# Kernel tuning notes

Hardware: AMD Instinct MI355X
Metric: run time of the kernel (lower is better)

Reference implementation:

```python
import jax, jax.numpy as jnp
import numpy as np

HIDDEN = 4544
NUM_HEADS = 71
HEAD_DIM = 64
SEQ = 2048
ROPE_BASE = 10000.0


def setup_inputs() -> dict:
    key = jax.random.key(0)
    k1, k2, k3 = jax.random.split(key, 3)
    hidden_states = jax.random.normal(k1, (1, 1, SEQ, HIDDEN), dtype=jnp.float32)
    # additive causal mask (0 on/below diagonal, -1e9 above)
    causal = jnp.tril(jnp.ones((SEQ, SEQ), dtype=bool))
    attention_mask = jnp.where(causal, 0.0, -1e9).astype(jnp.float32)[None, None]
    w_qkv = jax.random.normal(k2, (HIDDEN, (NUM_HEADS + 2) * HEAD_DIM), dtype=jnp.float32) * 0.02
    w_dense = jax.random.normal(k3, (HIDDEN, HIDDEN), dtype=jnp.float32) * 0.02
    # RoPE caches as in TtFalconRotaryEmbedding
    inv_freq = 1.0 / (ROPE_BASE ** (jnp.arange(0, HEAD_DIM, 2, dtype=jnp.float32) / HEAD_DIM))
    t = jnp.arange(SEQ, dtype=jnp.float32)
    freqs = jnp.outer(t, inv_freq)                      # [S, HD/2]
    emb = jnp.concatenate([freqs, freqs], axis=-1)      # [S, HD]
    return {
        "hidden_states": hidden_states,
        "attention_mask": attention_mask,
        "w_qkv": w_qkv,
        "w_dense": w_dense,
        "cos": jnp.cos(emb),
        "sin": jnp.sin(emb),
    }


def _rope(x, cos, sin):
    # x: [..., S, HD]; Falcon rotate_half: cat(-x2, x1)
    x1, x2 = jnp.split(x, 2, axis=-1)
    rot = jnp.concatenate([-x2, x1], axis=-1)
    return x * cos + rot * sin


def reference(hidden_states, attention_mask, w_qkv, w_dense, cos, sin):
    S = hidden_states.shape[2]
    x = hidden_states[0, 0]                              # [S, H]
    qkv = (x @ w_qkv).reshape(S, NUM_HEADS + 2, HEAD_DIM)
    q = jnp.transpose(qkv[:, :NUM_HEADS], (1, 0, 2))     # [nh, S, hd]
    k = qkv[:, NUM_HEADS]                                # [S, hd] (single MQA K head)
    v = qkv[:, NUM_HEADS + 1]                            # [S, hd]
    q = _rope(q, cos[None, :S], sin[None, :S])
    k = _rope(k, cos[:S], sin[:S])
    scale = 1.0 / np.sqrt(HEAD_DIM).astype(np.float32)
    scores = jnp.einsum('hsd,td->hst', q, k) * scale + attention_mask[0, 0][None]
    probs = jax.nn.softmax(scores, axis=-1)              # [nh, S, S]
    ctx = jnp.einsum('hst,td->hsd', probs, v)            # [nh, S, hd]
    out = jnp.transpose(ctx, (1, 0, 2)).reshape(S, NUM_HEADS * HEAD_DIM) @ w_dense
    return out[None, None]                               # [1, 1, S, H]
```

## Files before the change

kernel.cpp:

```cpp
#include <hip/hip_runtime.h>

typedef unsigned short u16;
typedef unsigned int u32;
typedef __attribute__((ext_vector_type(8))) __bf16 bf16x8;
typedef __attribute__((ext_vector_type(4))) float f32x4;

#define SEQ   2048
#define NH    71
#define HD    64
#define HID   4544
#define NQKV  4672
#define KP    4608
#define KSL   1536

__device__ __forceinline__ u16 f2bf(float f) {
    __bf16 b = (__bf16)f;
    return __builtin_bit_cast(u16, b);
}
__device__ __forceinline__ float bf2f(u16 u) {
    __bf16 b = __builtin_bit_cast(__bf16, u);
    return (float)b;
}

__device__ __forceinline__ void gload_lds16(const u16* g, u16* l) {
    __builtin_amdgcn_global_load_lds(
        (const __attribute__((address_space(1))) u32*)g,
        (__attribute__((address_space(3))) u32*)l, 16, 0, 0);
}

__global__ __launch_bounds__(256) void k_convert(const float* __restrict__ in,
                                                 u16* __restrict__ out) {
    const int row = blockIdx.x;
    const float* src = in + (size_t)row * HID;
    u16* dst = out + (size_t)row * KP;
    for (int c = threadIdx.x; c < KP / 8; c += 256) {
        u16 o[8];
        if (c < HID / 8) {
            float4 v0 = *(const float4*)(src + c * 8);
            float4 v1 = *(const float4*)(src + c * 8 + 4);
            o[0] = f2bf(v0.x); o[1] = f2bf(v0.y); o[2] = f2bf(v0.z); o[3] = f2bf(v0.w);
            o[4] = f2bf(v1.x); o[5] = f2bf(v1.y); o[6] = f2bf(v1.z); o[7] = f2bf(v1.w);
        } else {
#pragma unroll
            for (int j = 0; j < 8; ++j) o[j] = 0;
        }
        *(uint4*)(dst + c * 8) = *(uint4*)o;
    }
}

__global__ __launch_bounds__(256) void k_transpose(const float* __restrict__ in,
                                                   u16* __restrict__ out,
                                                   int R, int C, int Rp) {
    __shared__ float tile[32][33];
    int c0 = blockIdx.x * 32, r0 = blockIdx.y * 32;
    int tx = threadIdx.x & 31, ty = threadIdx.x >> 5;
#pragma unroll
    for (int i = 0; i < 32; i += 8) {
        int r = r0 + ty + i, c = c0 + tx;
        tile[ty + i][tx] = (r < R && c < C) ? in[(size_t)r * C + c] : 0.f;
    }
    __syncthreads();
#pragma unroll
    for (int i = 0; i < 32; i += 8)
        out[(size_t)(c0 + ty + i) * Rp + r0 + tx] = f2bf(tile[tx][ty + i]);
}

__global__ __launch_bounds__(512) void k_gemm_sk(const u16* __restrict__ A,
                                                 const u16* __restrict__ BT,
                                                 u16* __restrict__ C0,
                                                 u16* __restrict__ C1,
                                                 u16* __restrict__ C2,
                                                 int N, int ntN) {
    __shared__ u16 ls[4][256 * 64];
    const int tid = threadIdx.x;
    const int lane = tid & 63;
    const int wid = tid >> 6;
    const int wr = wid >> 2, wc = wid & 3;
    const int l15 = lane & 15, lg = lane >> 4;

    const int p = blockIdx.x;
    const int m0 = (p & 7) * 256;
    const int rr_ = p >> 3;
    const int ks = rr_ / ntN;
    const int n0 = (rr_ % ntN) * 256;
    const int k0 = ks * KSL;

    const int sg = lane >> 3;
    const int slot = lane & 7;
    const u16* sb[4];
    int dstoff[4];
#pragma unroll
    for (int i = 0; i < 4; ++i) {
        int r = i * 64 + wid * 8 + sg;
        int sc = slot ^ (r & 7);
        sb[i] = (sc < 4) ? (A  + (size_t)(m0 + r) * KP + k0 + sc * 8)
                         : (BT + (size_t)(n0 + r) * KP + k0 + (sc ^ 4) * 8);
        dstoff[i] = r * 64 + slot * 8;
    }

    f32x4 acc[8][4];
#pragma unroll
    for (int i = 0; i < 8; ++i)
#pragma unroll
        for (int j = 0; j < 4; ++j) acc[i][j] = (f32x4){0.f, 0.f, 0.f, 0.f};

#define STG(d, kt, i) gload_lds16(sb[i] + (size_t)(kt) * 32, &ls[d][dstoff[i]])

    const int NT = KSL / 32;
    STG(0, 0, 0); STG(0, 0, 1); STG(0, 0, 2); STG(0, 0, 3);
    STG(1, 1, 0); STG(1, 1, 1); STG(1, 1, 2); STG(1, 1, 3);
    STG(2, 2, 0); STG(2, 2, 1); STG(2, 2, 2); STG(2, 2, 3);
    asm volatile("s_waitcnt vmcnt(8)" ::: "memory");
    __builtin_amdgcn_s_barrier();

    for (int kt = 0; kt < NT; ++kt) {
        const u16* L = ls[kt & 3];
        const int db = (kt + 3) & 3;
        const bool st = (kt + 3 < NT);
        bf16x8 bfr[4], af[4];
#pragma unroll
        for (int ni = 0; ni < 4; ++ni) {
            int rb = wc * 64 + ni * 16 + l15;
            bfr[ni] = *(const bf16x8*)(L + rb * 64 + ((lg ^ (rb & 7) ^ 4) << 3));
        }
#pragma unroll
        for (int mi = 0; mi < 4; ++mi) {
            int ra = wr * 128 + mi * 16 + l15;
            af[mi] = *(const bf16x8*)(L + ra * 64 + ((lg ^ (ra & 7)) << 3));
        }
        if (st) { STG(db, kt + 3, 0); STG(db, kt + 3, 1); }
        __builtin_amdgcn_s_barrier();
        __builtin_amdgcn_s_setprio(1);
#pragma unroll
        for (int mi = 0; mi < 4; ++mi)
#pragma unroll
            for (int ni = 0; ni < 4; ++ni)
                acc[mi][ni] = __builtin_amdgcn_mfma_f32_16x16x32_bf16(
                    af[mi], bfr[ni], acc[mi][ni], 0, 0, 0);
        __builtin_amdgcn_s_setprio(0);
        __builtin_amdgcn_s_barrier();
#pragma unroll
        for (int mi = 0; mi < 4; ++mi) {
            int ra = wr * 128 + (mi + 4) * 16 + l15;
            af[mi] = *(const bf16x8*)(L + ra * 64 + ((lg ^ (ra & 7)) << 3));
        }
        if (st) { STG(db, kt + 3, 2); STG(db, kt + 3, 3); }
        __builtin_amdgcn_s_barrier();
        __builtin_amdgcn_s_setprio(1);
#pragma unroll
        for (int mi = 0; mi < 4; ++mi)
#pragma unroll
            for (int ni = 0; ni < 4; ++ni)
                acc[mi + 4][ni] = __builtin_amdgcn_mfma_f32_16x16x32_bf16(
                    af[mi], bfr[ni], acc[mi + 4][ni], 0, 0, 0);
        __builtin_amdgcn_s_setprio(0);
        if (kt < NT - 3)       asm volatile("s_waitcnt vmcnt(8)" ::: "memory");
        else if (kt == NT - 3) asm volatile("s_waitcnt vmcnt(4)" ::: "memory");
        else if (kt == NT - 2) asm volatile("s_waitcnt vmcnt(0)" ::: "memory");
        __builtin_amdgcn_s_barrier();
    }
#undef STG

    u16* Cks = (ks == 0) ? C0 : (ks == 1) ? C1 : C2;
#pragma unroll
    for (int mi = 0; mi < 8; ++mi)
#pragma unroll
        for (int ni = 0; ni < 4; ++ni) {
            int row = m0 + wr * 128 + mi * 16 + lg * 4;
            int col = n0 + wc * 64 + ni * 16 + l15;
            if (col < N) {
#pragma unroll
                for (int j = 0; j < 4; ++j)
                    Cks[(size_t)(row + j) * N + col] = f2bf(acc[mi][ni][j]);
            }
        }
}

__global__ __launch_bounds__(256) void k_reduce(const u16* __restrict__ P0,
                                                const u16* __restrict__ P1,
                                                const u16* __restrict__ P2,
                                                float* __restrict__ out, int n8) {
    for (int i = blockIdx.x * 256 + threadIdx.x; i < n8; i += gridDim.x * 256) {
        uint4 a = ((const uint4*)P0)[i];
        uint4 b = ((const uint4*)P1)[i];
        uint4 c = ((const uint4*)P2)[i];
        float r[8];
#pragma unroll
        for (int j = 0; j < 4; ++j) {
            u32 aw = (&a.x)[j], bw = (&b.x)[j], cw = (&c.x)[j];
            r[j * 2]     = bf2f((u16)(aw & 0xffff)) + bf2f((u16)(bw & 0xffff))
                         + bf2f((u16)(cw & 0xffff));
            r[j * 2 + 1] = bf2f((u16)(aw >> 16)) + bf2f((u16)(bw >> 16))
                         + bf2f((u16)(cw >> 16));
        }
        ((float4*)out)[i * 2]     = (float4){r[0], r[1], r[2], r[3]};
        ((float4*)out)[i * 2 + 1] = (float4){r[4], r[5], r[6], r[7]};
    }
}

__global__ __launch_bounds__(256) void k_rope(const u16* __restrict__ P0,
                                              const u16* __restrict__ P1,
                                              const u16* __restrict__ P2,
                                              const float* __restrict__ cosb,
                                              const float* __restrict__ sinb,
                                              u16* __restrict__ qb, u16* __restrict__ kb,
                                              u16* __restrict__ vT) {
    int s = blockIdx.x;
    __shared__ float row[NQKV];
    __shared__ float cs[64], sn[64];
    if (threadIdx.x < 64) {
        cs[threadIdx.x] = cosb[s * 64 + threadIdx.x];
        sn[threadIdx.x] = sinb[s * 64 + threadIdx.x];
    }
    const u16* r0 = P0 + (size_t)s * NQKV;
    const u16* r1 = P1 + (size_t)s * NQKV;
    const u16* r2 = P2 + (size_t)s * NQKV;
    for (int e = threadIdx.x; e < NQKV; e += 256)
        row[e] = bf2f(r0[e]) + bf2f(r1[e]) + bf2f(r2[e]);
    __syncthreads();
    const float qscale = 0.125f * 1.44269504f;
    for (int e = threadIdx.x; e < NQKV; e += 256) {
        int h = e >> 6, d = e & 63;
        float x = row[e];
        if (h < 72) {
            float other = row[h * 64 + ((d < 32) ? d + 32 : d - 32)];
            float rot = (d < 32) ? -other : other;
            float rr = x * cs[d] + rot * sn[d];
            if (h < NH) qb[((size_t)h * SEQ + s) * 64 + d] = f2bf(rr * qscale);
            else        kb[(size_t)s * 64 + d] = f2bf(rr);
        } else {
            vT[(size_t)d * SEQ + s] = f2bf(x);
        }
    }
}

__global__ __launch_bounds__(512) void k_attn(const u16* __restrict__ qb,
                                              const u16* __restrict__ kb,
                                              const u16* __restrict__ vT,
                                              u16* __restrict__ ctx) {
    const int tid = threadIdx.x;
    const int lane = tid & 63;
    const int wid = tid >> 6;
    const int l15 = lane & 15, lg = lane >> 4;

    const int bid = blockIdx.x;
    const int qt = 63 - bid / 9;
    const int hg = bid % 9;
    int h = hg * 8 + wid;
    const bool hval = (h < NH);
    if (!hval) h = NH - 1;
    const int q0 = qt * 32;
    const int nt = (qt >> 2) + 1;

    __shared__ u16 lsK[2][128 * 64];
    __shared__ u16 lsV[2][64 * 128];
    __shared__ u16 lsP[8][32 * 128];
    u16* myP = lsP[wid];

    const int kr = tid >> 3, kc = tid & 7;
    const int vd = tid >> 4, vc = tid & 15;

    bf16x8 qf[2][2];
#pragma unroll
    for (int mi = 0; mi < 2; ++mi)
#pragma unroll
        for (int ks = 0; ks < 2; ++ks)
            qf[mi][ks] = *(const bf16x8*)(qb + ((size_t)h * SEQ + q0 + mi * 16 + l15) * 64
                                          + ks * 32 + lg * 8);

    f32x4 oacc[2][4];
#pragma unroll
    for (int i = 0; i < 2; ++i)
#pragma unroll
        for (int j = 0; j < 4; ++j) oacc[i][j] = (f32x4){0.f, 0.f, 0.f, 0.f};
    float mrun[2] = {-3e38f, -3e38f};
    float lrun[2] = {0.f, 0.f};

    uint4 kg0, kg1, vg0, vg1;
    kg0 = *(const uint4*)(kb + (size_t)kr * 64 + kc * 8);
    kg1 = *(const uint4*)(kb + (size_t)(kr + 64) * 64 + kc * 8);
    vg0 = *(const uint4*)(vT + (size_t)vd * SEQ + vc * 8);
    vg1 = *(const uint4*)(vT + (size_t)(vd + 32) * SEQ + vc * 8);
    {
        const int kswz = (kr & 7) << 4;
        *(uint4*)((char*)lsK[0] + kr * 128 + ((kc * 16) ^ kswz)) = kg0;
        *(uint4*)((char*)lsK[0] + (kr + 64) * 128 + ((kc * 16) ^ kswz)) = kg1;
        *(uint4*)((char*)lsV[0] + vd * 256 + ((vc * 16) ^ ((vd & 15) << 4))) = vg0;
        *(uint4*)((char*)lsV[0] + (vd + 32) * 256 + ((vc * 16) ^ (((vd + 32) & 15) << 4))) = vg1;
    }

    for (int t = 0; t < nt; ++t) {
        const int t0 = t << 7;
        const int cb = t & 1;
        if (t + 1 < nt) {
            const int t1 = t0 + 128;
            kg0 = *(const uint4*)(kb + (size_t)(t1 + kr) * 64 + kc * 8);
            kg1 = *(const uint4*)(kb + (size_t)(t1 + kr + 64) * 64 + kc * 8);
            vg0 = *(const uint4*)(vT + (size_t)vd * SEQ + t1 + vc * 8);
            vg1 = *(const uint4*)(vT + (size_t)(vd + 32) * SEQ + t1 + vc * 8);
        }
        __syncthreads();

        f32x4 sacc[2][8];
#pragma unroll
        for (int i = 0; i < 2; ++i)
#pragma unroll
            for (int j = 0; j < 8; ++j) sacc[i][j] = (f32x4){0.f, 0.f, 0.f, 0.f};
        __builtin_amdgcn_s_setprio(1);
#pragma unroll
        for (int ni = 0; ni < 8; ++ni) {
            const int rr = ni * 16 + l15;
            const int swz = (rr & 7) << 4;
            bf16x8 kf0 = *(const bf16x8*)((const char*)lsK[cb] + rr * 128 + ((lg * 16) ^ swz));
            bf16x8 kf1 = *(const bf16x8*)((const char*)lsK[cb] + rr * 128 + ((64 + lg * 16) ^ swz));
            sacc[0][ni] = __builtin_amdgcn_mfma_f32_16x16x32_bf16(kf0, qf[0][0], sacc[0][ni], 0, 0, 0);
            sacc[1][ni] = __builtin_amdgcn_mfma_f32_16x16x32_bf16(kf0, qf[1][0], sacc[1][ni], 0, 0, 0);
            sacc[0][ni] = __builtin_amdgcn_mfma_f32_16x16x32_bf16(kf1, qf[0][1], sacc[0][ni], 0, 0, 0);
            sacc[1][ni] = __builtin_amdgcn_mfma_f32_16x16x32_bf16(kf1, qf[1][1], sacc[1][ni], 0, 0, 0);
        }
        __builtin_amdgcn_s_setprio(0);
        const bool last = (t == nt - 1);

#pragma unroll
        for (int mi = 0; mi < 2; ++mi) {
            const int q = q0 + mi * 16 + l15;
            if (last) {
#pragma unroll
                for (int ni = 0; ni < 8; ++ni)
#pragma unroll
                    for (int jj = 0; jj < 4; ++jj)
                        if (t0 + ni * 16 + lg * 4 + jj > q) sacc[mi][ni][jj] = -1e9f;
            }
            float m = sacc[mi][0][0];
#pragma unroll
            for (int ni = 0; ni < 8; ++ni)
#pragma unroll
                for (int jj = 0; jj < 4; ++jj) m = fmaxf(m, sacc[mi][ni][jj]);
            m = fmaxf(m, __shfl_xor(m, 16, 64));
            m = fmaxf(m, __shfl_xor(m, 32, 64));
            float mnew = fmaxf(mrun[mi], m);
            const bool skiprs = (__all(mnew - mrun[mi] <= 8.0f) != 0);
            float mref = skiprs ? mrun[mi] : mnew;
            float rs = 0.f;
#pragma unroll
            for (int ni = 0; ni < 8; ++ni)
#pragma unroll
                for (int jj = 0; jj < 4; ++jj) {
                    float pp = exp2f(sacc[mi][ni][jj] - mref);
                    sacc[mi][ni][jj] = pp;
                    rs += pp;
                }
            rs += __shfl_xor(rs, 16, 64);
            rs += __shfl_xor(rs, 32, 64);
            if (skiprs) {
                lrun[mi] += rs;
            } else {
                float alpha = exp2f(mrun[mi] - mnew);
                lrun[mi] = lrun[mi] * alpha + rs;
                mrun[mi] = mnew;
#pragma unroll
                for (int jj = 0; jj < 4; ++jj) {
                    float aB = __shfl(alpha, (lane & 48) + ((lane >> 4) & 3) * 4 + jj, 64);
#pragma unroll
                    for (int nd = 0; nd < 4; ++nd) oacc[mi][nd][jj] *= aB;
                }
            }

            const int qh = mi * 16 + l15;
            const int pswz = (qh & 7) << 4;
#pragma unroll
            for (int ni = 0; ni < 8; ++ni) {
                u32 w0 = (u32)f2bf(sacc[mi][ni][0]) | ((u32)f2bf(sacc[mi][ni][1]) << 16);
                u32 w1 = (u32)f2bf(sacc[mi][ni][2]) | ((u32)f2bf(sacc[mi][ni][3]) << 16);
                uint2 w; w.x = w0; w.y = w1;
                *(uint2*)((char*)myP + qh * 256 + ((ni * 32 + lg * 8) ^ pswz)) = w;
            }
        }

        __builtin_amdgcn_s_setprio(1);
#pragma unroll
        for (int ks = 0; ks < 4; ++ks) {
            bf16x8 pf[2];
#pragma unroll
            for (int mi = 0; mi < 2; ++mi) {
                const int qh = mi * 16 + l15;
                pf[mi] = *(const bf16x8*)((const char*)myP + qh * 256
                                          + ((ks * 64 + lg * 16) ^ ((qh & 7) << 4)));
            }
#pragma unroll
            for (int nd = 0; nd < 4; ++nd) {
                const int rr = nd * 16 + l15;
                bf16x8 vf = *(const bf16x8*)((const char*)lsV[cb] + rr * 256
                                             + ((ks * 64 + lg * 16) ^ ((rr & 15) << 4)));
                oacc[0][nd] = __builtin_amdgcn_mfma_f32_16x16x32_bf16(pf[0], vf, oacc[0][nd], 0, 0, 0);
                oacc[1][nd] = __builtin_amdgcn_mfma_f32_16x16x32_bf16(pf[1], vf, oacc[1][nd], 0, 0, 0);
            }
        }
        __builtin_amdgcn_s_setprio(0);

        if (t + 1 < nt) {
            const int nb = cb ^ 1;
            const int kswz = (kr & 7) << 4;
            *(uint4*)((char*)lsK[nb] + kr * 128 + ((kc * 16) ^ kswz)) = kg0;
            *(uint4*)((char*)lsK[nb] + (kr + 64) * 128 + ((kc * 16) ^ kswz)) = kg1;
            *(uint4*)((char*)lsV[nb] + vd * 256 + ((vc * 16) ^ ((vd & 15) << 4))) = vg0;
            *(uint4*)((char*)lsV[nb] + (vd + 32) * 256 + ((vc * 16) ^ (((vd + 32) & 15) << 4))) = vg1;
        }
    }

    if (hval) {
#pragma unroll
        for (int mi = 0; mi < 2; ++mi)
#pragma unroll
            for (int jj = 0; jj < 4; ++jj) {
                float lB = __shfl(lrun[mi], (lane & 48) + ((lane >> 4) & 3) * 4 + jj, 64);
                float inv = 1.0f / lB;
                int q = q0 + mi * 16 + lg * 4 + jj;
#pragma unroll
                for (int nd = 0; nd < 4; ++nd)
                    ctx[(size_t)q * KP + h * 64 + nd * 16 + l15] = f2bf(oacc[mi][nd][jj] * inv);
            }
    } else {
#pragma unroll
        for (int mi = 0; mi < 2; ++mi)
#pragma unroll
            for (int jj = 0; jj < 4; ++jj) {
                int q = q0 + mi * 16 + lg * 4 + jj;
#pragma unroll
                for (int nd = 0; nd < 4; ++nd)
                    ctx[(size_t)q * KP + HID + nd * 16 + l15] = 0;
            }
    }
}

extern "C" void kernel_launch(void* const* d_in, const int* in_sizes, int n_in,
                              void* d_out, int out_size, void* d_ws, size_t ws_size,
                              hipStream_t stream) {
    const float* hs      = (const float*)d_in[0];
    const float* w_qkv   = (const float*)d_in[2];
    const float* w_dense = (const float*)d_in[3];
    const float* cosb    = (const float*)d_in[4];
    const float* sinb    = (const float*)d_in[5];
    float* out = (float*)d_out;

    char* ws = (char*)d_ws;
    u16*   x_bf  = (u16*)(ws + 0);
    u16*   wT    = (u16*)(ws + 18874368);
    u16*   qP0   = (u16*)(ws + 63700992);
    u16*   qP1   = (u16*)(ws + 82837504);
    u16*   qP2   = (u16*)(ws + 101974016);
    u16*   q_bf  = (u16*)(ws + 121110528);
    u16*   k_bf  = (u16*)(ws + 139722752);
    u16*   vT_bf = (u16*)(ws + 139984896);
    u16*   dP0   = (u16*)(ws + 63700992);
    u16*   dP1   = (u16*)(ws + 82837504);
    u16*   dP2   = (u16*)(ws + 101974016);

    k_convert<<<2048, 256, 0, stream>>>(hs, x_bf);
    k_transpose<<<dim3(152, 144), 256, 0, stream>>>(w_qkv, wT, HID, NQKV, KP);
    k_gemm_sk<<<dim3(456), 512, 0, stream>>>(x_bf, wT, qP0, qP1, qP2, NQKV, 19);
    k_rope<<<SEQ, 256, 0, stream>>>(qP0, qP1, qP2, cosb, sinb, q_bf, k_bf, vT_bf);
    k_attn<<<dim3(576), 512, 0, stream>>>(q_bf, k_bf, vT_bf, x_bf );
    k_transpose<<<dim3(144, 144), 256, 0, stream>>>(w_dense, wT, HID, HID, KP);
    k_gemm_sk<<<dim3(432), 512, 0, stream>>>(x_bf , wT, dP0, dP1, dP2, HID, 18);
    k_reduce<<<2048, 256, 0, stream>>>(dP0, dP1, dP2, out, SEQ * HID / 8);
}
```

Before: 406.9 us.

## Single-buffer K/V tiles and shrink per-wave P scratch in attention kernel

```diff
diff --git a/kernel.cpp b/kernel.cpp
--- a/kernel.cpp
+++ b/kernel.cpp
@@ -252,9 +252,9 @@
     const int q0 = qt * 32;
     const int nt = (qt >> 2) + 1;
 
-    __shared__ u16 lsK[2][128 * 64];
-    __shared__ u16 lsV[2][64 * 128];
-    __shared__ u16 lsP[8][32 * 128];
+    __shared__ u16 lsK[128 * 64];
+    __shared__ u16 lsV[64 * 128];
+    __shared__ u16 lsP[8][16 * 128];
     u16* myP = lsP[wid];
 
     const int kr = tid >> 3, kc = tid & 7;
@@ -276,30 +276,28 @@
     float mrun[2] = {-3e38f, -3e38f};
     float lrun[2] = {0.f, 0.f};
 
+    const int kswz = (kr & 7) << 4;
     uint4 kg0, kg1, vg0, vg1;
     kg0 = *(const uint4*)(kb + (size_t)kr * 64 + kc * 8);
     kg1 = *(const uint4*)(kb + (size_t)(kr + 64) * 64 + kc * 8);
     vg0 = *(const uint4*)(vT + (size_t)vd * SEQ + vc * 8);
     vg1 = *(const uint4*)(vT + (size_t)(vd + 32) * SEQ + vc * 8);
-    {
-        const int kswz = (kr & 7) << 4;
-        *(uint4*)((char*)lsK[0] + kr * 128 + ((kc * 16) ^ kswz)) = kg0;
-        *(uint4*)((char*)lsK[0] + (kr + 64) * 128 + ((kc * 16) ^ kswz)) = kg1;
-        *(uint4*)((char*)lsV[0] + vd * 256 + ((vc * 16) ^ ((vd & 15) << 4))) = vg0;
-        *(uint4*)((char*)lsV[0] + (vd + 32) * 256 + ((vc * 16) ^ (((vd + 32) & 15) << 4))) = vg1;
-    }
+    *(uint4*)((char*)lsK + kr * 128 + ((kc * 16) ^ kswz)) = kg0;
+    *(uint4*)((char*)lsK + (kr + 64) * 128 + ((kc * 16) ^ kswz)) = kg1;
+    *(uint4*)((char*)lsV + vd * 256 + ((vc * 16) ^ ((vd & 15) << 4))) = vg0;
+    *(uint4*)((char*)lsV + (vd + 32) * 256 + ((vc * 16) ^ (((vd + 32) & 15) << 4))) = vg1;
+    __syncthreads();
 
     for (int t = 0; t < nt; ++t) {
         const int t0 = t << 7;
-        const int cb = t & 1;
-        if (t + 1 < nt) {
+        const bool more = (t + 1 < nt);
+        if (more) {
             const int t1 = t0 + 128;
             kg0 = *(const uint4*)(kb + (size_t)(t1 + kr) * 64 + kc * 8);
             kg1 = *(const uint4*)(kb + (size_t)(t1 + kr + 64) * 64 + kc * 8);
             vg0 = *(const uint4*)(vT + (size_t)vd * SEQ + t1 + vc * 8);
             vg1 = *(const uint4*)(vT + (size_t)(vd + 32) * SEQ + t1 + vc * 8);
         }
-        __syncthreads();
 
         f32x4 sacc[2][8];
 #pragma unroll
@@ -311,8 +309,8 @@
         for (int ni = 0; ni < 8; ++ni) {
             const int rr = ni * 16 + l15;
             const int swz = (rr & 7) << 4;
-            bf16x8 kf0 = *(const bf16x8*)((const char*)lsK[cb] + rr * 128 + ((lg * 16) ^ swz));
-            bf16x8 kf1 = *(const bf16x8*)((const char*)lsK[cb] + rr * 128 + ((64 + lg * 16) ^ swz));
+            bf16x8 kf0 = *(const bf16x8*)((const char*)lsK + rr * 128 + ((lg * 16) ^ swz));
+            bf16x8 kf1 = *(const bf16x8*)((const char*)lsK + rr * 128 + ((64 + lg * 16) ^ swz));
             sacc[0][ni] = __builtin_amdgcn_mfma_f32_16x16x32_bf16(kf0, qf[0][0], sacc[0][ni], 0, 0, 0);
             sacc[1][ni] = __builtin_amdgcn_mfma_f32_16x16x32_bf16(kf0, qf[1][0], sacc[1][ni], 0, 0, 0);
             sacc[0][ni] = __builtin_amdgcn_mfma_f32_16x16x32_bf16(kf1, qf[0][1], sacc[0][ni], 0, 0, 0);
@@ -321,6 +319,7 @@
         __builtin_amdgcn_s_setprio(0);
         const bool last = (t == nt - 1);
 
+        const int pswz = (l15 & 7) << 4;
 #pragma unroll
         for (int mi = 0; mi < 2; ++mi) {
             const int q = q0 + mi * 16 + l15;
@@ -366,45 +365,38 @@
                 }
             }
 
-            const int qh = mi * 16 + l15;
-            const int pswz = (qh & 7) << 4;
 #pragma unroll
             for (int ni = 0; ni < 8; ++ni) {
                 u32 w0 = (u32)f2bf(sacc[mi][ni][0]) | ((u32)f2bf(sacc[mi][ni][1]) << 16);
                 u32 w1 = (u32)f2bf(sacc[mi][ni][2]) | ((u32)f2bf(sacc[mi][ni][3]) << 16);
                 uint2 w; w.x = w0; w.y = w1;
-                *(uint2*)((char*)myP + qh * 256 + ((ni * 32 + lg * 8) ^ pswz)) = w;
-            }
-        }
-
-        __builtin_amdgcn_s_setprio(1);
-#pragma unroll
-        for (int ks = 0; ks < 4; ++ks) {
-            bf16x8 pf[2];
-#pragma unroll
-            for (int mi = 0; mi < 2; ++mi) {
-                const int qh = mi * 16 + l15;
-                pf[mi] = *(const bf16x8*)((const char*)myP + qh * 256
-                                          + ((ks * 64 + lg * 16) ^ ((qh & 7) << 4)));
-            }
-#pragma unroll
-            for (int nd = 0; nd < 4; ++nd) {
-                const int rr = nd * 16 + l15;
-                bf16x8 vf = *(const bf16x8*)((const char*)lsV[cb] + rr * 256
-                                             + ((ks * 64 + lg * 16) ^ ((rr & 15) << 4)));
-                oacc[0][nd] = __builtin_amdgcn_mfma_f32_16x16x32_bf16(pf[0], vf, oacc[0][nd], 0, 0, 0);
-                oacc[1][nd] = __builtin_amdgcn_mfma_f32_16x16x32_bf16(pf[1], vf, oacc[1][nd], 0, 0, 0);
-            }
-        }
-        __builtin_amdgcn_s_setprio(0);
-
-        if (t + 1 < nt) {
-            const int nb = cb ^ 1;
-            const int kswz = (kr & 7) << 4;
-            *(uint4*)((char*)lsK[nb] + kr * 128 + ((kc * 16) ^ kswz)) = kg0;
-            *(uint4*)((char*)lsK[nb] + (kr + 64) * 128 + ((kc * 16) ^ kswz)) = kg1;
-            *(uint4*)((char*)lsV[nb] + vd * 256 + ((vc * 16) ^ ((vd & 15) << 4))) = vg0;
-            *(uint4*)((char*)lsV[nb] + (vd + 32) * 256 + ((vc * 16) ^ (((vd + 32) & 15) << 4))) = vg1;
+                *(uint2*)((char*)myP + l15 * 256 + ((ni * 32 + lg * 8) ^ pswz)) = w;
+            }
+
+            __builtin_amdgcn_s_setprio(1);
+#pragma unroll
+            for (int ks = 0; ks < 4; ++ks) {
+                bf16x8 pf = *(const bf16x8*)((const char*)myP + l15 * 256
+                                             + ((ks * 64 + lg * 16) ^ pswz));
+#pragma unroll
+                for (int nd = 0; nd < 4; ++nd) {
+                    const int rr = nd * 16 + l15;
+                    bf16x8 vf = *(const bf16x8*)((const char*)lsV + rr * 256
+                                                 + ((ks * 64 + lg * 16) ^ ((rr & 15) << 4)));
+                    oacc[mi][nd] = __builtin_amdgcn_mfma_f32_16x16x32_bf16(
+                        pf, vf, oacc[mi][nd], 0, 0, 0);
+                }
+            }
+            __builtin_amdgcn_s_setprio(0);
+        }
+
+        if (more) {
+            __syncthreads();
+            *(uint4*)((char*)lsK + kr * 128 + ((kc * 16) ^ kswz)) = kg0;
+            *(uint4*)((char*)lsK + (kr + 64) * 128 + ((kc * 16) ^ kswz)) = kg1;
+            *(uint4*)((char*)lsV + vd * 256 + ((vc * 16) ^ ((vd & 15) << 4))) = vg0;
+            *(uint4*)((char*)lsV + (vd + 32) * 256 + ((vc * 16) ^ (((vd + 32) & 15) << 4))) = vg1;
+            __syncthreads();
         }
     }
 
```

New measurement: 418.4 us. +2.8%, slower.
